# Optimization experiments

Measured on AMD Instinct MI355X. Metric: run time of the kernel, lower is better.

The kernel has to match this reference:

```python
import jax, jax.numpy as jnp
import numpy as np

B, S, H, I, E = 4, 4096, 1024, 4096, 4
VOCAB = 32000


def setup_inputs() -> dict:
    key = jax.random.key(0)
    k1, k2, k3, k4, k5 = jax.random.split(key, 5)
    scale = 1.0 / np.sqrt(H)
    return {
        "hidden_states": jax.random.normal(k1, (B, S, H), dtype=jnp.float32),
        "gate_proj": jax.random.normal(k2, (E, H, I), dtype=jnp.float32) * scale,
        "up_proj": jax.random.normal(k3, (E, H, I), dtype=jnp.float32) * scale,
        "down_proj": jax.random.normal(k4, (E, I, H), dtype=jnp.float32) * (1.0 / np.sqrt(I)),
        "token_ids": jax.random.randint(k5, (B, S), 0, VOCAB, dtype=jnp.int64),
    }


def reference(hidden_states, gate_proj, up_proj, down_proj, token_ids):
    # hidden_states: [B, S, H]; token_ids: [B, S]
    num_experts = gate_proj.shape[0]
    expert_ids = token_ids % num_experts  # [B, S]
    out = jnp.zeros_like(hidden_states)
    for e in range(num_experts):  # small fixed expert loop
        gate = jax.nn.silu(jnp.einsum("bsh,hi->bsi", hidden_states, gate_proj[e]))
        up = jnp.einsum("bsh,hi->bsi", hidden_states, up_proj[e])
        y = jnp.einsum("bsi,ih->bsh", gate * up, down_proj[e])
        out = jnp.where((expert_ids == e)[..., None], y, out)
    return out
```

## Files before the change

kernel.cpp:

```cpp
#include <hip/hip_runtime.h>

#define TOK   16384
#define HD    1024
#define ID    4096
#define NE    4
#define MAXMT 131

typedef __attribute__((ext_vector_type(4))) float f32x4;
typedef __attribute__((ext_vector_type(8))) short bf16x8;

static __device__ __forceinline__ unsigned short f2bf(float f) {
  unsigned u = __float_as_uint(f);
  u += 0x7FFFu + ((u >> 16) & 1u);
  return (unsigned short)(u >> 16);
}

__global__ void k_route0(const int* __restrict__ ids, int* __restrict__ meta) {
  __shared__ int cnt[4];
  int t = threadIdx.x;
  if (t < 4) cnt[t] = 0;
  __syncthreads();
  int l0 = 0, l1 = 0, l2 = 0, l3 = 0;
  for (int i = t; i < TOK; i += 256) {
    int e = ids[i] & 3;
    l0 += (e == 0); l1 += (e == 1); l2 += (e == 2); l3 += (e == 3);
  }
  atomicAdd(&cnt[0], l0); atomicAdd(&cnt[1], l1);
  atomicAdd(&cnt[2], l2); atomicAdd(&cnt[3], l3);
  __syncthreads();
  if (t == 0) {
    int o = 0;
    for (int e = 0; e < 4; ++e) { meta[e] = o; meta[8 + e] = o; o += cnt[e]; }
    meta[4] = o;
  }
}

__global__ void k_route1(const int* __restrict__ ids, int* __restrict__ meta,
                         int* __restrict__ perm) {
  int i = blockIdx.x * 256 + threadIdx.x;
  if (i < TOK) {
    int e = ids[i] & 3;
    int s = atomicAdd(&meta[8 + e], 1);
    perm[s] = i;
  }
}

__global__ void k_conv(const float* __restrict__ s, unsigned short* __restrict__ d, int n8) {
  int i = blockIdx.x * blockDim.x + threadIdx.x;
  int st = gridDim.x * blockDim.x;
  for (; i < n8; i += st) {
    const f32x4* p = (const f32x4*)(s + ((size_t)i << 3));
    f32x4 a = p[0], b = p[1];
    union { unsigned short u[8]; uint4 q; } o;
    o.u[0] = f2bf(a.x); o.u[1] = f2bf(a.y); o.u[2] = f2bf(a.z); o.u[3] = f2bf(a.w);
    o.u[4] = f2bf(b.x); o.u[5] = f2bf(b.y); o.u[6] = f2bf(b.z); o.u[7] = f2bf(b.w);
    *(uint4*)(d + ((size_t)i << 3)) = o.q;
  }
}

__global__ void k_tr(const float* __restrict__ src, unsigned short* __restrict__ dst,
                     int R, int C) {
  __shared__ float tile[64][65];
  size_t mo = (size_t)blockIdx.z * R * C;
  const float* s = src + mo;
  unsigned short* d = dst + mo;
  int r0 = blockIdx.y << 6, c0 = blockIdx.x << 6;
  int t = threadIdx.x;
  int lr = t >> 4, lc = (t & 15) << 2;
  #pragma unroll
  for (int it = 0; it < 4; ++it) {
    int r = lr + (it << 4);
    f32x4 v = *(const f32x4*)(s + (size_t)(r0 + r) * C + c0 + lc);
    tile[r][lc] = v.x; tile[r][lc + 1] = v.y; tile[r][lc + 2] = v.z; tile[r][lc + 3] = v.w;
  }
  __syncthreads();
  int c = t >> 2, rb = (t & 3) << 4;
  union { unsigned short u[16]; uint4 q[2]; } o;
  #pragma unroll
  for (int j = 0; j < 16; ++j) o.u[j] = f2bf(tile[rb + j][c]);
  uint4* dp = (uint4*)(d + (size_t)(c0 + c) * R + r0 + rb);
  dp[0] = o.q[0]; dp[1] = o.q[1];
}

__global__ __launch_bounds__(256, 2) void k_gemm1(
    const unsigned short* __restrict__ hid,
    const unsigned short* __restrict__ gT,
    const unsigned short* __restrict__ uT,
    const int* __restrict__ meta,
    const int* __restrict__ perm,
    unsigned short* __restrict__ act) {
  __shared__ unsigned short As[128 * 64];
  __shared__ unsigned short Gs[128 * 64];
  __shared__ unsigned short Us[128 * 64];
  int offs[5];
  #pragma unroll
  for (int i = 0; i < 5; ++i) offs[i] = meta[i];
  int mt = blockIdx.x;
  int e = -1, mloc = 0, base = 0;
  #pragma unroll
  for (int ee = 0; ee < 4; ++ee) {
    int tiles = (offs[ee + 1] - offs[ee] + 127) >> 7;
    if (e < 0 && mt < base + tiles) { e = ee; mloc = mt - base; }
    base += tiles;
  }
  if (e < 0) return;
  int slot0 = offs[e] + (mloc << 7);
  int send = offs[e + 1];
  int tid = threadIdx.x;
  int n0 = blockIdx.y << 7;
  const unsigned short* gbase = gT + (size_t)e * ID * HD;
  const unsigned short* ubase = uT + (size_t)e * ID * HD;
  const unsigned short* ap[4];
  const unsigned short* gp[4];
  const unsigned short* up[4];
  int wofs[4];
  #pragma unroll
  for (int it = 0; it < 4; ++it) {
    int b = (tid << 4) + (it << 12);
    int row = b >> 7;
    int kob = b & 127;
    int slot = slot0 + row;
    int pr = perm[slot < send ? slot : slot0];
    ap[it] = hid + (size_t)pr * HD + (kob >> 1);
    gp[it] = gbase + (size_t)(n0 + row) * HD + (kob >> 1);
    up[it] = ubase + (size_t)(n0 + row) * HD + (kob >> 1);
    wofs[it] = row * 64 + ((kob ^ ((row & 7) << 4)) >> 1);
  }
  int lane = tid & 63, wid = tid >> 6;
  int wm = wid >> 1, wn = wid & 1;
  int r16 = lane & 15, kg = lane >> 4;
  f32x4 zero = {0.f, 0.f, 0.f, 0.f};
  f32x4 ag[4][4], au[4][4];
  #pragma unroll
  for (int m = 0; m < 4; ++m)
    #pragma unroll
    for (int n = 0; n < 4; ++n) { ag[m][n] = zero; au[m][n] = zero; }

  bf16x8 sa[4], sg[4], su[4];
  #pragma unroll
  for (int it = 0; it < 4; ++it) {
    sa[it] = *(const bf16x8*)(ap[it]);
    sg[it] = *(const bf16x8*)(gp[it]);
    su[it] = *(const bf16x8*)(up[it]);
  }
  for (int kt = 0; kt < HD / 64; ++kt) {
    __syncthreads();
    #pragma unroll
    for (int it = 0; it < 4; ++it) {
      *(bf16x8*)(As + wofs[it]) = sa[it];
      *(bf16x8*)(Gs + wofs[it]) = sg[it];
      *(bf16x8*)(Us + wofs[it]) = su[it];
    }
    __syncthreads();
    if (kt < HD / 64 - 1) {
      int ko = (kt + 1) << 6;
      #pragma unroll
      for (int it = 0; it < 4; ++it) {
        sa[it] = *(const bf16x8*)(ap[it] + ko);
        sg[it] = *(const bf16x8*)(gp[it] + ko);
        su[it] = *(const bf16x8*)(up[it] + ko);
      }
    }
    #pragma unroll
    for (int kk = 0; kk < 2; ++kk) {
      bf16x8 fa[4], fg[4], fu[4];
      #pragma unroll
      for (int m = 0; m < 4; ++m) {
        int row = (wm << 6) + (m << 4) + r16;
        int kob = (kk << 6) + (kg << 4);
        fa[m] = *(const bf16x8*)(As + row * 64 + ((kob ^ ((row & 7) << 4)) >> 1));
      }
      #pragma unroll
      for (int n = 0; n < 4; ++n) {
        int row = (wn << 6) + (n << 4) + r16;
        int kob = (kk << 6) + (kg << 4);
        int o2 = row * 64 + ((kob ^ ((row & 7) << 4)) >> 1);
        fg[n] = *(const bf16x8*)(Gs + o2);
        fu[n] = *(const bf16x8*)(Us + o2);
      }
      #pragma unroll
      for (int m = 0; m < 4; ++m)
        #pragma unroll
        for (int n = 0; n < 4; ++n) {
          ag[m][n] = __builtin_amdgcn_mfma_f32_16x16x32_bf16(fa[m], fg[n], ag[m][n], 0, 0, 0);
          au[m][n] = __builtin_amdgcn_mfma_f32_16x16x32_bf16(fa[m], fu[n], au[m][n], 0, 0, 0);
        }
    }
  }
  #pragma unroll
  for (int m = 0; m < 4; ++m) {
    int lr = (wm << 6) + (m << 4) + (kg << 2);
    #pragma unroll
    for (int n = 0; n < 4; ++n) {
      int col = n0 + (wn << 6) + (n << 4) + r16;
      #pragma unroll
      for (int r = 0; r < 4; ++r) {
        int slot = slot0 + lr + r;
        if (slot < send) {
          float g = ag[m][n][r];
          float u = au[m][n][r];
          float y = (g / (1.f + __expf(-g))) * u;
          act[(size_t)slot * ID + col] = f2bf(y);
        }
      }
    }
  }
}

__global__ __launch_bounds__(256, 2) void k_gemm2(
    const unsigned short* __restrict__ act,
    const unsigned short* __restrict__ dT,
    const int* __restrict__ meta,
    const int* __restrict__ perm,
    float* __restrict__ out) {
  __shared__ unsigned short As[128 * 64];
  __shared__ unsigned short Bs[128 * 64];
  int offs[5];
  #pragma unroll
  for (int i = 0; i < 5; ++i) offs[i] = meta[i];
  int mt = blockIdx.x;
  int e = -1, mloc = 0, base = 0;
  #pragma unroll
  for (int ee = 0; ee < 4; ++ee) {
    int tiles = (offs[ee + 1] - offs[ee] + 127) >> 7;
    if (e < 0 && mt < base + tiles) { e = ee; mloc = mt - base; }
    base += tiles;
  }
  if (e < 0) return;
  int slot0 = offs[e] + (mloc << 7);
  int send = offs[e + 1];
  int tid = threadIdx.x;
  int n0 = blockIdx.y << 7;
  const unsigned short* dbase = dT + (size_t)e * HD * ID;
  const unsigned short* ap[4];
  const unsigned short* bp[4];
  int wofs[4];
  #pragma unroll
  for (int it = 0; it < 4; ++it) {
    int b = (tid << 4) + (it << 12);
    int row = b >> 7;
    int kob = b & 127;
    int slot = slot0 + row;
    int s2 = slot < send ? slot : slot0;
    ap[it] = act + (size_t)s2 * ID + (kob >> 1);
    bp[it] = dbase + (size_t)(n0 + row) * ID + (kob >> 1);
    wofs[it] = row * 64 + ((kob ^ ((row & 7) << 4)) >> 1);
  }
  int lane = tid & 63, wid = tid >> 6;
  int wm = wid >> 1, wn = wid & 1;
  int r16 = lane & 15, kg = lane >> 4;
  f32x4 zero = {0.f, 0.f, 0.f, 0.f};
  f32x4 acc[4][4];
  #pragma unroll
  for (int m = 0; m < 4; ++m)
    #pragma unroll
    for (int n = 0; n < 4; ++n) acc[m][n] = zero;

  bf16x8 sa[4], sb[4];
  #pragma unroll
  for (int it = 0; it < 4; ++it) {
    sa[it] = *(const bf16x8*)(ap[it]);
    sb[it] = *(const bf16x8*)(bp[it]);
  }
  for (int kt = 0; kt < ID / 64; ++kt) {
    __syncthreads();
    #pragma unroll
    for (int it = 0; it < 4; ++it) {
      *(bf16x8*)(As + wofs[it]) = sa[it];
      *(bf16x8*)(Bs + wofs[it]) = sb[it];
    }
    __syncthreads();
    if (kt < ID / 64 - 1) {
      int ko = (kt + 1) << 6;
      #pragma unroll
      for (int it = 0; it < 4; ++it) {
        sa[it] = *(const bf16x8*)(ap[it] + ko);
        sb[it] = *(const bf16x8*)(bp[it] + ko);
      }
    }
    #pragma unroll
    for (int kk = 0; kk < 2; ++kk) {
      bf16x8 fa[4], fb[4];
      #pragma unroll
      for (int m = 0; m < 4; ++m) {
        int row = (wm << 6) + (m << 4) + r16;
        int kob = (kk << 6) + (kg << 4);
        fa[m] = *(const bf16x8*)(As + row * 64 + ((kob ^ ((row & 7) << 4)) >> 1));
      }
      #pragma unroll
      for (int n = 0; n < 4; ++n) {
        int row = (wn << 6) + (n << 4) + r16;
        int kob = (kk << 6) + (kg << 4);
        fb[n] = *(const bf16x8*)(Bs + row * 64 + ((kob ^ ((row & 7) << 4)) >> 1));
      }
      #pragma unroll
      for (int m = 0; m < 4; ++m)
        #pragma unroll
        for (int n = 0; n < 4; ++n)
          acc[m][n] = __builtin_amdgcn_mfma_f32_16x16x32_bf16(fa[m], fb[n], acc[m][n], 0, 0, 0);
    }
  }
  #pragma unroll
  for (int m = 0; m < 4; ++m) {
    int lr = (wm << 6) + (m << 4) + (kg << 2);
    int pr4[4];
    #pragma unroll
    for (int r = 0; r < 4; ++r) {
      int slot = slot0 + lr + r;
      pr4[r] = slot < send ? perm[slot] : -1;
    }
    #pragma unroll
    for (int n = 0; n < 4; ++n) {
      int col = n0 + (wn << 6) + (n << 4) + r16;
      #pragma unroll
      for (int r = 0; r < 4; ++r) {
        if (pr4[r] >= 0) out[(size_t)pr4[r] * HD + col] = acc[m][n][r];
      }
    }
  }
}

extern "C" void kernel_launch(void* const* d_in, const int* in_sizes, int n_in,
                              void* d_out, int out_size, void* d_ws, size_t ws_size,
                              hipStream_t stream) {
  const float* hs = (const float*)d_in[0];
  const float* gw = (const float*)d_in[1];
  const float* uw = (const float*)d_in[2];
  const float* dw = (const float*)d_in[3];
  const int* ids = (const int*)d_in[4];
  float* out = (float*)d_out;

  char* w = (char*)d_ws;
  size_t o = 0;
  int* meta = (int*)(w + o); o += 64;
  int* perm = (int*)(w + o); o += (size_t)TOK * 4;
  o = (o + 255) & ~(size_t)255;
  unsigned short* hid = (unsigned short*)(w + o); o += (size_t)TOK * HD * 2;
  unsigned short* gT  = (unsigned short*)(w + o); o += (size_t)NE * ID * HD * 2;
  unsigned short* uT  = (unsigned short*)(w + o); o += (size_t)NE * ID * HD * 2;
  unsigned short* dT  = (unsigned short*)(w + o); o += (size_t)NE * ID * HD * 2;
  unsigned short* actb = (unsigned short*)(w + o); o += (size_t)TOK * ID * 2;

  hipLaunchKernelGGL(k_route0, dim3(1), dim3(256), 0, stream, ids, meta);
  hipLaunchKernelGGL(k_route1, dim3(TOK / 256), dim3(256), 0, stream, ids, meta, perm);
  hipLaunchKernelGGL(k_conv, dim3(2048), dim3(256), 0, stream, hs, hid, TOK * HD / 8);
  hipLaunchKernelGGL(k_tr, dim3(ID / 64, HD / 64, NE), dim3(256), 0, stream, gw, gT, HD, ID);
  hipLaunchKernelGGL(k_tr, dim3(ID / 64, HD / 64, NE), dim3(256), 0, stream, uw, uT, HD, ID);
  hipLaunchKernelGGL(k_tr, dim3(HD / 64, ID / 64, NE), dim3(256), 0, stream, dw, dT, ID, HD);
  hipLaunchKernelGGL(k_gemm1, dim3(MAXMT, ID / 128), dim3(256), 0, stream,
                     hid, gT, uT, meta, perm, actb);
  hipLaunchKernelGGL(k_gemm2, dim3(MAXMT, HD / 128), dim3(256), 0, stream,
                     actb, dT, meta, perm, out);
}
```

Measured before the change: 731.9 us.

## Rewrite gate/up GEMM with 256-row tiles, async LDS loads and double buffering

The gate/up GEMM kernel now uses 512 threads with 256-row M tiles, 128 KB of dynamic LDS and two buffers. Global-to-LDS copies use the direct global_load_lds builtin and are prefetched one K step ahead, with explicit vmcnt waits. The MFMA phases are split around raw barriers and raised wave priority. This removes the register staging round trip and overlaps memory with compute, at the cost of one block per CU given the LDS size and a more fragile hand-written synchronisation scheme.

```diff
diff --git a/kernel.cpp b/kernel.cpp
--- a/kernel.cpp
+++ b/kernel.cpp
@@ -1,18 +1,31 @@
 #include <hip/hip_runtime.h>
 
-#define TOK   16384
-#define HD    1024
-#define ID    4096
-#define NE    4
-#define MAXMT 131
+#define TOK    16384
+#define HD     1024
+#define ID     4096
+#define NE     4
+#define MAXMT  131
+#define MAXMT2 67
 
 typedef __attribute__((ext_vector_type(4))) float f32x4;
 typedef __attribute__((ext_vector_type(8))) short bf16x8;
+typedef unsigned int u32;
 
 static __device__ __forceinline__ unsigned short f2bf(float f) {
   unsigned u = __float_as_uint(f);
   u += 0x7FFFu + ((u >> 16) & 1u);
   return (unsigned short)(u >> 16);
+}
+
+static __device__ __forceinline__ void gl16(const void* g, void* l) {
+  __builtin_amdgcn_global_load_lds((const __attribute__((address_space(1))) u32*)g,
+                                   (__attribute__((address_space(3))) u32*)l, 16, 0, 0);
+}
+
+static __device__ __forceinline__ void barx() {
+  asm volatile("" ::: "memory");
+  __builtin_amdgcn_s_barrier();
+  asm volatile("" ::: "memory");
 }
 
 __global__ void k_route0(const int* __restrict__ ids, int* __restrict__ meta) {
@@ -82,16 +95,16 @@
   dp[0] = o.q[0]; dp[1] = o.q[1];
 }
 
-__global__ __launch_bounds__(256, 2) void k_gemm1(
+#define MFMA16 __builtin_amdgcn_mfma_f32_16x16x32_bf16
+
+__global__ __launch_bounds__(512, 2) void k_gemm1(
     const unsigned short* __restrict__ hid,
     const unsigned short* __restrict__ gT,
     const unsigned short* __restrict__ uT,
     const int* __restrict__ meta,
     const int* __restrict__ perm,
     unsigned short* __restrict__ act) {
-  __shared__ unsigned short As[128 * 64];
-  __shared__ unsigned short Gs[128 * 64];
-  __shared__ unsigned short Us[128 * 64];
+  extern __shared__ __align__(16) char smem[];
   int offs[5];
   #pragma unroll
   for (int i = 0; i < 5; ++i) offs[i] = meta[i];
@@ -99,36 +112,58 @@
   int e = -1, mloc = 0, base = 0;
   #pragma unroll
   for (int ee = 0; ee < 4; ++ee) {
-    int tiles = (offs[ee + 1] - offs[ee] + 127) >> 7;
+    int tiles = (offs[ee + 1] - offs[ee] + 255) >> 8;
     if (e < 0 && mt < base + tiles) { e = ee; mloc = mt - base; }
     base += tiles;
   }
   if (e < 0) return;
-  int slot0 = offs[e] + (mloc << 7);
+  int slot0 = offs[e] + (mloc << 8);
   int send = offs[e + 1];
-  int tid = threadIdx.x;
+  int tid = threadIdx.x, lane = tid & 63, wid = tid >> 6;
   int n0 = blockIdx.y << 7;
-  const unsigned short* gbase = gT + (size_t)e * ID * HD;
-  const unsigned short* ubase = uT + (size_t)e * ID * HD;
-  const unsigned short* ap[4];
-  const unsigned short* gp[4];
-  const unsigned short* up[4];
-  int wofs[4];
-  #pragma unroll
-  for (int it = 0; it < 4; ++it) {
-    int b = (tid << 4) + (it << 12);
-    int row = b >> 7;
-    int kob = b & 127;
-    int slot = slot0 + row;
+
+  int ke = (((tid & 7) ^ ((tid >> 3) & 7)) << 3);
+  int rloc = tid >> 3;
+  const unsigned short* srcA[4];
+  #pragma unroll
+  for (int i = 0; i < 4; ++i) {
+    int slot = slot0 + i * 64 + rloc;
     int pr = perm[slot < send ? slot : slot0];
-    ap[it] = hid + (size_t)pr * HD + (kob >> 1);
-    gp[it] = gbase + (size_t)(n0 + row) * HD + (kob >> 1);
-    up[it] = ubase + (size_t)(n0 + row) * HD + (kob >> 1);
-    wofs[it] = row * 64 + ((kob ^ ((row & 7) << 4)) >> 1);
-  }
-  int lane = tid & 63, wid = tid >> 6;
+    srcA[i] = hid + (size_t)pr * HD + ke;
+  }
+  const unsigned short* gb = gT + (size_t)e * ID * HD;
+  const unsigned short* ub = uT + (size_t)e * ID * HD;
+  const unsigned short* srcG[2];
+  const unsigned short* srcU[2];
+  #pragma unroll
+  for (int i = 0; i < 2; ++i) {
+    int row = n0 + i * 64 + rloc;
+    srcG[i] = gb + (size_t)row * HD + ke;
+    srcU[i] = ub + (size_t)row * HD + ke;
+  }
+  int dstA[4], dstG[2], dstU[2];
+  #pragma unroll
+  for (int i = 0; i < 4; ++i) dstA[i] = i * 8192 + wid * 1024;
+  #pragma unroll
+  for (int i = 0; i < 2; ++i) { dstG[i] = 32768 + i * 8192 + wid * 1024;
+                                dstU[i] = 49152 + i * 8192 + wid * 1024; }
+
   int wm = wid >> 1, wn = wid & 1;
   int r16 = lane & 15, kg = lane >> 4;
+  int offA[4], offG[4], offU[4];
+  #pragma unroll
+  for (int m = 0; m < 4; ++m) {
+    int row = wm * 64 + m * 16 + r16;
+    offA[m] = row * 128 + ((kg << 4) ^ ((row & 7) << 4));
+  }
+  #pragma unroll
+  for (int n = 0; n < 4; ++n) {
+    int row = wn * 64 + n * 16 + r16;
+    int o = row * 128 + ((kg << 4) ^ ((row & 7) << 4));
+    offG[n] = 32768 + o;
+    offU[n] = 49152 + o;
+  }
+
   f32x4 zero = {0.f, 0.f, 0.f, 0.f};
   f32x4 ag[4][4], au[4][4];
   #pragma unroll
@@ -136,63 +171,99 @@
     #pragma unroll
     for (int n = 0; n < 4; ++n) { ag[m][n] = zero; au[m][n] = zero; }
 
-  bf16x8 sa[4], sg[4], su[4];
-  #pragma unroll
-  for (int it = 0; it < 4; ++it) {
-    sa[it] = *(const bf16x8*)(ap[it]);
-    sg[it] = *(const bf16x8*)(gp[it]);
-    su[it] = *(const bf16x8*)(up[it]);
-  }
-  for (int kt = 0; kt < HD / 64; ++kt) {
-    __syncthreads();
-    #pragma unroll
-    for (int it = 0; it < 4; ++it) {
-      *(bf16x8*)(As + wofs[it]) = sa[it];
-      *(bf16x8*)(Gs + wofs[it]) = sg[it];
-      *(bf16x8*)(Us + wofs[it]) = su[it];
-    }
-    __syncthreads();
-    if (kt < HD / 64 - 1) {
-      int ko = (kt + 1) << 6;
-      #pragma unroll
-      for (int it = 0; it < 4; ++it) {
-        sa[it] = *(const bf16x8*)(ap[it] + ko);
-        sg[it] = *(const bf16x8*)(gp[it] + ko);
-        su[it] = *(const bf16x8*)(up[it] + ko);
-      }
-    }
-    #pragma unroll
-    for (int kk = 0; kk < 2; ++kk) {
-      bf16x8 fa[4], fg[4], fu[4];
-      #pragma unroll
-      for (int m = 0; m < 4; ++m) {
-        int row = (wm << 6) + (m << 4) + r16;
-        int kob = (kk << 6) + (kg << 4);
-        fa[m] = *(const bf16x8*)(As + row * 64 + ((kob ^ ((row & 7) << 4)) >> 1));
-      }
-      #pragma unroll
-      for (int n = 0; n < 4; ++n) {
-        int row = (wn << 6) + (n << 4) + r16;
-        int kob = (kk << 6) + (kg << 4);
-        int o2 = row * 64 + ((kob ^ ((row & 7) << 4)) >> 1);
-        fg[n] = *(const bf16x8*)(Gs + o2);
-        fu[n] = *(const bf16x8*)(Us + o2);
-      }
-      #pragma unroll
-      for (int m = 0; m < 4; ++m)
-        #pragma unroll
-        for (int n = 0; n < 4; ++n) {
-          ag[m][n] = __builtin_amdgcn_mfma_f32_16x16x32_bf16(fa[m], fg[n], ag[m][n], 0, 0, 0);
-          au[m][n] = __builtin_amdgcn_mfma_f32_16x16x32_bf16(fa[m], fu[n], au[m][n], 0, 0, 0);
-        }
-    }
-  }
+  {
+    char* b = smem;
+    #pragma unroll
+    for (int i = 0; i < 4; ++i) gl16(srcA[i], b + dstA[i]);
+    #pragma unroll
+    for (int i = 0; i < 2; ++i) gl16(srcG[i], b + dstG[i]);
+    #pragma unroll
+    for (int i = 0; i < 2; ++i) gl16(srcU[i], b + dstU[i]);
+  }
+
+  #pragma unroll 2
+  for (int t = 0; t < HD / 64; ++t) {
+    const char* bc = smem + (t & 1) * 65536;
+    if (t < HD / 64 - 1) {
+      char* bn = smem + ((t + 1) & 1) * 65536;
+      int ko = (t + 1) * 64;
+      #pragma unroll
+      for (int i = 0; i < 4; ++i) gl16(srcA[i] + ko, bn + dstA[i]);
+      #pragma unroll
+      for (int i = 0; i < 2; ++i) gl16(srcG[i] + ko, bn + dstG[i]);
+      #pragma unroll
+      for (int i = 0; i < 2; ++i) gl16(srcU[i] + ko, bn + dstU[i]);
+      asm volatile("s_waitcnt vmcnt(8)" ::: "memory");
+    } else {
+      asm volatile("s_waitcnt vmcnt(0)" ::: "memory");
+    }
+    barx();
+
+    bf16x8 fa[4], fg[4], fu[4];
+    #pragma unroll
+    for (int m = 0; m < 4; ++m) fa[m] = *(const bf16x8*)(bc + offA[m]);
+    #pragma unroll
+    for (int n = 0; n < 4; ++n) fg[n] = *(const bf16x8*)(bc + offG[n]);
+    barx();
+    asm volatile("s_waitcnt lgkmcnt(0)" ::: "memory");
+    __builtin_amdgcn_sched_barrier(0);
+    __builtin_amdgcn_s_setprio(1);
+    #pragma unroll
+    for (int m = 0; m < 4; ++m)
+      #pragma unroll
+      for (int n = 0; n < 4; ++n)
+        ag[m][n] = MFMA16(fa[m], fg[n], ag[m][n], 0, 0, 0);
+    __builtin_amdgcn_s_setprio(0);
+    barx();
+    #pragma unroll
+    for (int n = 0; n < 4; ++n) fu[n] = *(const bf16x8*)(bc + offU[n]);
+    barx();
+    asm volatile("s_waitcnt lgkmcnt(0)" ::: "memory");
+    __builtin_amdgcn_sched_barrier(0);
+    __builtin_amdgcn_s_setprio(1);
+    #pragma unroll
+    for (int m = 0; m < 4; ++m)
+      #pragma unroll
+      for (int n = 0; n < 4; ++n)
+        au[m][n] = MFMA16(fa[m], fu[n], au[m][n], 0, 0, 0);
+    __builtin_amdgcn_s_setprio(0);
+    barx();
+    #pragma unroll
+    for (int m = 0; m < 4; ++m) fa[m] = *(const bf16x8*)(bc + (offA[m] ^ 64));
+    #pragma unroll
+    for (int n = 0; n < 4; ++n) fg[n] = *(const bf16x8*)(bc + (offG[n] ^ 64));
+    barx();
+    asm volatile("s_waitcnt lgkmcnt(0)" ::: "memory");
+    __builtin_amdgcn_sched_barrier(0);
+    __builtin_amdgcn_s_setprio(1);
+    #pragma unroll
+    for (int m = 0; m < 4; ++m)
+      #pragma unroll
+      for (int n = 0; n < 4; ++n)
+        ag[m][n] = MFMA16(fa[m], fg[n], ag[m][n], 0, 0, 0);
+    __builtin_amdgcn_s_setprio(0);
+    barx();
+    #pragma unroll
+    for (int n = 0; n < 4; ++n) fu[n] = *(const bf16x8*)(bc + (offU[n] ^ 64));
+    barx();
+    asm volatile("s_waitcnt lgkmcnt(0)" ::: "memory");
+    __builtin_amdgcn_sched_barrier(0);
+    __builtin_amdgcn_s_setprio(1);
+    #pragma unroll
+    for (int m = 0; m < 4; ++m)
+      #pragma unroll
+      for (int n = 0; n < 4; ++n)
+        au[m][n] = MFMA16(fa[m], fu[n], au[m][n], 0, 0, 0);
+    __builtin_amdgcn_s_setprio(0);
+    barx();
+  }
+
   #pragma unroll
   for (int m = 0; m < 4; ++m) {
-    int lr = (wm << 6) + (m << 4) + (kg << 2);
+    int lr = wm * 64 + m * 16 + kg * 4;
     #pragma unroll
     for (int n = 0; n < 4; ++n) {
-      int col = n0 + (wn << 6) + (n << 4) + r16;
+      int col = n0 + wn * 64 + n * 16 + r16;
       #pragma unroll
       for (int r = 0; r < 4; ++r) {
         int slot = slot0 + lr + r;
@@ -341,13 +412,16 @@
   unsigned short* dT  = (unsigned short*)(w + o); o += (size_t)NE * ID * HD * 2;
   unsigned short* actb = (unsigned short*)(w + o); o += (size_t)TOK * ID * 2;
 
+  hipFuncSetAttribute((const void*)k_gemm1,
+                      hipFuncAttributeMaxDynamicSharedMemorySize, 131072);
+
   hipLaunchKernelGGL(k_route0, dim3(1), dim3(256), 0, stream, ids, meta);
   hipLaunchKernelGGL(k_route1, dim3(TOK / 256), dim3(256), 0, stream, ids, meta, perm);
   hipLaunchKernelGGL(k_conv, dim3(2048), dim3(256), 0, stream, hs, hid, TOK * HD / 8);
   hipLaunchKernelGGL(k_tr, dim3(ID / 64, HD / 64, NE), dim3(256), 0, stream, gw, gT, HD, ID);
   hipLaunchKernelGGL(k_tr, dim3(ID / 64, HD / 64, NE), dim3(256), 0, stream, uw, uT, HD, ID);
   hipLaunchKernelGGL(k_tr, dim3(HD / 64, ID / 64, NE), dim3(256), 0, stream, dw, dT, ID, HD);
-  hipLaunchKernelGGL(k_gemm1, dim3(MAXMT, ID / 128), dim3(256), 0, stream,
+  hipLaunchKernelGGL(k_gemm1, dim3(MAXMT2, ID / 128), dim3(512), 131072, stream,
                      hid, gT, uT, meta, perm, actb);
   hipLaunchKernelGGL(k_gemm2, dim3(MAXMT, HD / 128), dim3(256), 0, stream,
                      actb, dT, meta, perm, out);
```

New measurement: 767.7 us. +4.9%, slower.

## Merge weight transposes into one launch, remap GEMM block order per XCD, raise occupancy

Applied to the files above, without the earlier changes.

The three weight-transpose launches become one kernel that picks gate, up or down weights from blockIdx.y. Both GEMMs switch to a 1D grid whose block index is remapped so that consecutive blocks on the same XCD (bid&7) share an M-tile across N-tiles, improving L2 reuse of the activation rows. Launch bounds rise from 2 to 3 waves-per-SIMD blocks, which may force register pressure or spills. MAXMT*32 and MAXMT*8 both divide by 8, so the remap is a bijection over the logical tile space.

```diff
diff --git a/kernel.cpp b/kernel.cpp
--- a/kernel.cpp
+++ b/kernel.cpp
@@ -1,10 +1,10 @@
 #include <hip/hip_runtime.h>
 
-#define TOK   16384
-#define HD    1024
-#define ID    4096
-#define NE    4
-#define MAXMT 131
+#define TOK    16384
+#define HD     1024
+#define ID     4096
+#define NE     4
+#define MAXMT  131
 
 typedef __attribute__((ext_vector_type(4))) float f32x4;
 typedef __attribute__((ext_vector_type(8))) short bf16x8;
@@ -58,13 +58,25 @@
   }
 }
 
-__global__ void k_tr(const float* __restrict__ src, unsigned short* __restrict__ dst,
-                     int R, int C) {
+__global__ void k_tr12(const float* __restrict__ gw, const float* __restrict__ uw,
+                       const float* __restrict__ dw, unsigned short* __restrict__ gT,
+                       unsigned short* __restrict__ uT, unsigned short* __restrict__ dT) {
   __shared__ float tile[64][65];
-  size_t mo = (size_t)blockIdx.z * R * C;
-  const float* s = src + mo;
-  unsigned short* d = dst + mo;
-  int r0 = blockIdx.y << 6, c0 = blockIdx.x << 6;
+  int z = blockIdx.y;
+  const float* s; unsigned short* d; int R, C, lg;
+  if (z < 8) {
+    R = HD; C = ID; lg = 6;
+    int m = z & 3;
+    if (z < 4) { s = gw + (size_t)m * R * C; d = gT + (size_t)m * R * C; }
+    else       { s = uw + (size_t)m * R * C; d = uT + (size_t)m * R * C; }
+  } else {
+    R = ID; C = HD; lg = 4;
+    int m = z - 8;
+    s = dw + (size_t)m * R * C; d = dT + (size_t)m * R * C;
+  }
+  int bx = blockIdx.x;
+  int tx = bx & ((1 << lg) - 1), ty = bx >> lg;
+  int r0 = ty << 6, c0 = tx << 6;
   int t = threadIdx.x;
   int lr = t >> 4, lc = (t & 15) << 2;
   #pragma unroll
@@ -82,7 +94,7 @@
   dp[0] = o.q[0]; dp[1] = o.q[1];
 }
 
-__global__ __launch_bounds__(256, 2) void k_gemm1(
+__global__ __launch_bounds__(256, 3) void k_gemm1(
     const unsigned short* __restrict__ hid,
     const unsigned short* __restrict__ gT,
     const unsigned short* __restrict__ uT,
@@ -95,7 +107,10 @@
   int offs[5];
   #pragma unroll
   for (int i = 0; i < 5; ++i) offs[i] = meta[i];
-  int mt = blockIdx.x;
+  int bid = blockIdx.x;
+  int logical = (bid & 7) * (MAXMT * 32 / 8) + (bid >> 3);
+  int mt = logical >> 5;
+  int ny = logical & 31;
   int e = -1, mloc = 0, base = 0;
   #pragma unroll
   for (int ee = 0; ee < 4; ++ee) {
@@ -107,7 +122,7 @@
   int slot0 = offs[e] + (mloc << 7);
   int send = offs[e + 1];
   int tid = threadIdx.x;
-  int n0 = blockIdx.y << 7;
+  int n0 = ny << 7;
   const unsigned short* gbase = gT + (size_t)e * ID * HD;
   const unsigned short* ubase = uT + (size_t)e * ID * HD;
   const unsigned short* ap[4];
@@ -207,7 +222,7 @@
   }
 }
 
-__global__ __launch_bounds__(256, 2) void k_gemm2(
+__global__ __launch_bounds__(256, 3) void k_gemm2(
     const unsigned short* __restrict__ act,
     const unsigned short* __restrict__ dT,
     const int* __restrict__ meta,
@@ -218,7 +233,10 @@
   int offs[5];
   #pragma unroll
   for (int i = 0; i < 5; ++i) offs[i] = meta[i];
-  int mt = blockIdx.x;
+  int bid = blockIdx.x;
+  int logical = (bid & 7) * (MAXMT * 8 / 8) + (bid >> 3);
+  int mt = logical >> 3;
+  int nyy = logical & 7;
   int e = -1, mloc = 0, base = 0;
   #pragma unroll
   for (int ee = 0; ee < 4; ++ee) {
@@ -230,7 +248,7 @@
   int slot0 = offs[e] + (mloc << 7);
   int send = offs[e + 1];
   int tid = threadIdx.x;
-  int n0 = blockIdx.y << 7;
+  int n0 = nyy << 7;
   const unsigned short* dbase = dT + (size_t)e * HD * ID;
   const unsigned short* ap[4];
   const unsigned short* bp[4];
@@ -344,11 +362,9 @@
   hipLaunchKernelGGL(k_route0, dim3(1), dim3(256), 0, stream, ids, meta);
   hipLaunchKernelGGL(k_route1, dim3(TOK / 256), dim3(256), 0, stream, ids, meta, perm);
   hipLaunchKernelGGL(k_conv, dim3(2048), dim3(256), 0, stream, hs, hid, TOK * HD / 8);
-  hipLaunchKernelGGL(k_tr, dim3(ID / 64, HD / 64, NE), dim3(256), 0, stream, gw, gT, HD, ID);
-  hipLaunchKernelGGL(k_tr, dim3(ID / 64, HD / 64, NE), dim3(256), 0, stream, uw, uT, HD, ID);
-  hipLaunchKernelGGL(k_tr, dim3(HD / 64, ID / 64, NE), dim3(256), 0, stream, dw, dT, ID, HD);
-  hipLaunchKernelGGL(k_gemm1, dim3(MAXMT, ID / 128), dim3(256), 0, stream,
+  hipLaunchKernelGGL(k_tr12, dim3(1024, 12), dim3(256), 0, stream, gw, uw, dw, gT, uT, dT);
+  hipLaunchKernelGGL(k_gemm1, dim3(MAXMT * 32), dim3(256), 0, stream,
                      hid, gT, uT, meta, perm, actb);
-  hipLaunchKernelGGL(k_gemm2, dim3(MAXMT, HD / 128), dim3(256), 0, stream,
+  hipLaunchKernelGGL(k_gemm2, dim3(MAXMT * 8), dim3(256), 0, stream,
                      actb, dT, meta, perm, out);
 }
```

Result: slower. 1.538 ms (+110.2%).
